# Kernel tuning notes

Hardware: AMD Instinct MI355X
Metric: run time of the kernel (lower is better)

Reference implementation:

```python
import jax, jax.numpy as jnp
import numpy as np

B_, N, C, H = 2048, 49, 384, 12
WH, WW = 7, 7
HEAD_DIM = C // H
SCALE = HEAD_DIM ** -0.5
TABLE = (2 * WH - 1) * (2 * WW - 1)  # 169


def _relative_position_index():
    coords = np.stack(np.meshgrid(np.arange(WH), np.arange(WW), indexing='ij'))  # [2,Wh,Ww]
    flat = coords.reshape(2, -1)  # [2,N]
    rel = flat[:, :, None] - flat[:, None, :]  # [2,N,N]
    rel = rel.transpose(1, 2, 0).astype(np.int32)  # [N,N,2]
    rel[:, :, 0] += WH - 1
    rel[:, :, 1] += WW - 1
    rel[:, :, 0] *= 2 * WW - 1
    return rel.sum(-1)  # [N,N] int32 in [0,169)


def setup_inputs() -> dict:
    key = jax.random.key(0)
    ks = jax.random.split(key, 8)
    return {
        'x': jax.random.normal(ks[0], (B_, N, C), jnp.float32),
        'mask': jax.random.normal(ks[1], (B_, 1, N, N), jnp.float32),
        'stagein': jax.random.uniform(ks[2], (B_, N, C), jnp.float32),
        'rel_bias_table': jax.random.normal(ks[3], (TABLE, H), jnp.float32) * 0.02,
        'rel_pos_index': jnp.asarray(_relative_position_index()),
        'qkv_w': jax.random.normal(ks[4], (3 * C, C), jnp.float32) * 0.02,
        'qkv_b': jax.random.normal(ks[5], (3 * C,), jnp.float32) * 0.02,
        'proj_w': jax.random.normal(ks[6], (C, C), jnp.float32) * 0.02,
        'proj_b': jax.random.normal(ks[7], (C,), jnp.float32) * 0.02,
    }


def reference(x, mask, stagein, rel_bias_table, rel_pos_index, qkv_w, qkv_b, proj_w, proj_b):
    x = x * stagein  # stagein is not None branch
    qkv = x @ qkv_w.T + qkv_b  # [B_, N, 3C]
    qkv = qkv.reshape(B_, N, 3, H, HEAD_DIM).transpose(2, 0, 3, 1, 4)  # [3,B_,H,N,hd]
    q, k, v = qkv[0], qkv[1], qkv[2]
    q = q * SCALE
    attn = jnp.einsum('bhnd,bhmd->bhnm', q, k)  # [B_,H,N,N]
    # relative position bias gather: [N*N] -> [N,N,H] -> [1,H,N,N]
    bias = rel_bias_table[rel_pos_index.reshape(-1)].reshape(N, N, H)
    bias = bias.transpose(2, 0, 1)[None]
    attn = jax.nn.softmax(attn + bias + mask, axis=-1)
    out = jnp.einsum('bhnm,bhmd->bhnd', attn, v)  # [B_,H,N,hd]
    out = out.transpose(0, 2, 1, 3).reshape(B_, N, C)
    return out @ proj_w.T + proj_b
```

## Files before the change

kernel.cpp:

```cpp
#include <hip/hip_runtime.h>
#include <hip/hip_bf16.h>
#include <stdint.h>

#define NWIN 2048
#define NTOK 49
#define CDIM 384
#define NHEAD 12
#define HD 32
#define C3 1152
#define NN2 2401
#define MROWS 100352

typedef __bf16 bf16x8 __attribute__((ext_vector_type(8)));
typedef float f32x4 __attribute__((ext_vector_type(4)));
typedef uint32_t u32x4 __attribute__((ext_vector_type(4)));

static __device__ __forceinline__ unsigned short f2bf(float f) {
  uint32_t u = __builtin_bit_cast(uint32_t, f);
  u += 0x7fffu + ((u >> 16) & 1u);
  return (unsigned short)(u >> 16);
}

static __device__ __forceinline__ void gload_lds16(const void* g, void* l) {
  __builtin_amdgcn_global_load_lds((const __attribute__((address_space(1))) void*)g,
                                   (__attribute__((address_space(3))) void*)l,
                                   16, 0, 0);
}

static __device__ __forceinline__ bf16x8 zero8() {
  u32x4 z = {0u, 0u, 0u, 0u};
  return __builtin_bit_cast(bf16x8, z);
}

__global__ void prep_kernel(const float* __restrict__ qkv_w, const float* __restrict__ proj_w,
                            const float* __restrict__ table, const int* __restrict__ idx,
                            unsigned short* __restrict__ wq, unsigned short* __restrict__ wp,
                            float* __restrict__ biasexp) {
  const int NW1 = C3 * CDIM;
  const int NW2 = CDIM * CDIM;
  const int NB = NHEAD * NN2;
  int i = blockIdx.x * blockDim.x + threadIdx.x;
  int stride = gridDim.x * blockDim.x;
  for (int t = i; t < NW1 + NW2 + NB; t += stride) {
    if (t < NW1) {
      wq[t] = f2bf(qkv_w[t]);
    } else if (t < NW1 + NW2) {
      int j = t - NW1;
      wp[j] = f2bf(proj_w[j]);
    } else {
      int j = t - NW1 - NW2;
      int h = j / NN2;
      int nm = j - h * NN2;
      biasexp[j] = table[idx[nm] * NHEAD + h];
    }
  }
}

__global__ void mul_kernel(const float4* __restrict__ x, const float4* __restrict__ s,
                           u32x4* __restrict__ A, int n8) {
  int i0 = blockIdx.x * blockDim.x + threadIdx.x;
  int stride = gridDim.x * blockDim.x;
  for (int t = i0; t < n8; t += stride) {
    float4 a0 = x[2 * t], a1 = x[2 * t + 1];
    float4 b0 = s[2 * t], b1 = s[2 * t + 1];
    union { unsigned short us[8]; u32x4 v; } o;
    o.us[0] = f2bf(a0.x * b0.x); o.us[1] = f2bf(a0.y * b0.y);
    o.us[2] = f2bf(a0.z * b0.z); o.us[3] = f2bf(a0.w * b0.w);
    o.us[4] = f2bf(a1.x * b1.x); o.us[5] = f2bf(a1.y * b1.y);
    o.us[6] = f2bf(a1.z * b1.z); o.us[7] = f2bf(a1.w * b1.w);
    A[t] = o.v;
  }
}

__launch_bounds__(256, 2)
__global__ void qkv_gemm(const unsigned short* __restrict__ A,
                         const unsigned short* __restrict__ Bw,
                         const float* __restrict__ qkvb,
                         unsigned short* __restrict__ qo,
                         unsigned short* __restrict__ ko,
                         unsigned short* __restrict__ vo) {
  __shared__ unsigned short As[128 * 64];
  __shared__ unsigned short Bs[128 * 64];
  const int tid = threadIdx.x;
  const int w = tid >> 6, l = tid & 63;
  const int l15 = l & 15, lhi = l >> 4;
  const int wgid = (blockIdx.x & 7) * 882 + (blockIdx.x >> 3);
  const int mt = wgid / 9, nt = wgid - mt * 9;
  const int wr = w >> 1, wc = w & 1;
  const int srow = tid >> 3;
  const int scb = (tid & 7) ^ (srow & 7);
  const unsigned short* Ag = A + (size_t)(mt * 128 + srow) * CDIM + scb * 8;
  const unsigned short* Bg = Bw + (size_t)(nt * 128 + srow) * CDIM + scb * 8;
  unsigned short* Asl = As + srow * 64 + (tid & 7) * 8;
  unsigned short* Bsl = Bs + srow * 64 + (tid & 7) * 8;
  const f32x4 z4 = {0.f, 0.f, 0.f, 0.f};
  f32x4 acc[4][4];
#pragma unroll
  for (int m = 0; m < 4; ++m)
#pragma unroll
    for (int n = 0; n < 4; ++n) acc[m][n] = z4;
  const int xr = l15 & 7;
  for (int kt = 0; kt < 6; ++kt) {
    const unsigned short* ag = Ag + kt * 64;
    const unsigned short* bg = Bg + kt * 64;
#pragma unroll
    for (int i = 0; i < 4; ++i) {
      gload_lds16(ag + i * 32 * CDIM, Asl + i * 2048);
      gload_lds16(bg + i * 32 * CDIM, Bsl + i * 2048);
    }
    __syncthreads();
#pragma unroll
    for (int kk = 0; kk < 2; ++kk) {
      const int sl = ((kk << 2) | lhi) ^ xr;
      bf16x8 af[4], bfr[4];
#pragma unroll
      for (int m = 0; m < 4; ++m)
        af[m] = *(const bf16x8*)(As + (wr * 64 + m * 16 + l15) * 64 + sl * 8);
#pragma unroll
      for (int n = 0; n < 4; ++n)
        bfr[n] = *(const bf16x8*)(Bs + (wc * 64 + n * 16 + l15) * 64 + sl * 8);
#pragma unroll
      for (int m = 0; m < 4; ++m)
#pragma unroll
        for (int n = 0; n < 4; ++n)
          acc[m][n] = __builtin_amdgcn_mfma_f32_16x16x32_bf16(af[m], bfr[n], acc[m][n], 0, 0, 0);
    }
    __syncthreads();
  }
  const float SCALE_F = 0.17677669529663687f;
  const int six = nt * 2 + wc;
  const int which = six / 6;
  const int cbase = (six - which * 6) * 64;
  unsigned short* outw = (which == 0) ? qo : ((which == 1) ? ko : vo);
  const float* bptr = qkvb + which * CDIM;
#pragma unroll
  for (int m = 0; m < 4; ++m) {
#pragma unroll
    for (int j = 0; j < 4; ++j) {
      const int r = mt * 128 + wr * 64 + m * 16 + lhi * 4 + j;
      const int bwin = r / 49;
      const int ntok = r - bwin * 49;
#pragma unroll
      for (int n = 0; n < 4; ++n) {
        const int c = cbase + n * 16 + l15;
        const int h = c >> 5, d = c & 31;
        float val = acc[m][n][j] + bptr[c];
        if (which == 0) val *= SCALE_F;
        outw[(((size_t)bwin * NHEAD + h) * NTOK + ntok) * HD + d] = f2bf(val);
      }
    }
  }
}

__launch_bounds__(256, 2)
__global__ void attn_kernel(const unsigned short* __restrict__ q,
                            const unsigned short* __restrict__ kmat,
                            const unsigned short* __restrict__ vmat,
                            const float* __restrict__ mask,
                            const float* __restrict__ biasexp,
                            unsigned short* __restrict__ attnout) {
  __shared__ unsigned short P_lds[4][64 * 72];
  __shared__ unsigned short vT_lds[4][32 * 72];
  const int tid = threadIdx.x;
  const int w = tid >> 6, l = tid & 63;
  const int l15 = l & 15, lhi = l >> 4;
  const int wg = (blockIdx.x & 7) * 768 + (blockIdx.x >> 3);
  const int b = wg / 3, it = wg - b * 3;
  unsigned short* Pw = &P_lds[w][0];
  unsigned short* Vw = &vT_lds[w][0];
  const float* maskb = mask + (size_t)b * NN2;
  const f32x4 z4 = {0.f, 0.f, 0.f, 0.f};
  const int h = it * 4 + w;
  const size_t hb = ((size_t)b * NHEAD + h) * NTOK * HD;
  const unsigned short* qb = q + hb;
  const unsigned short* kb = kmat + hb;
  const unsigned short* vb = vmat + hb;
  {
    const int n = l;
    unsigned short tmp[32];
    if (n < 49) {
      *(u32x4*)(&tmp[0])  = *(const u32x4*)(vb + n * 32);
      *(u32x4*)(&tmp[8])  = *(const u32x4*)(vb + n * 32 + 8);
      *(u32x4*)(&tmp[16]) = *(const u32x4*)(vb + n * 32 + 16);
      *(u32x4*)(&tmp[24]) = *(const u32x4*)(vb + n * 32 + 24);
    } else {
#pragma unroll
      for (int d2 = 0; d2 < 32; ++d2) tmp[d2] = 0;
    }
#pragma unroll
    for (int d2 = 0; d2 < 32; ++d2) Vw[d2 * 72 + n] = tmp[d2];
  }
  bf16x8 aq[4], bk[4];
#pragma unroll
  for (int t = 0; t < 4; ++t) {
    const int row = t * 16 + l15;
    if (row < 49) {
      aq[t] = *(const bf16x8*)(qb + row * 32 + lhi * 8);
      bk[t] = *(const bf16x8*)(kb + row * 32 + lhi * 8);
    } else {
      aq[t] = zero8();
      bk[t] = zero8();
    }
  }
  f32x4 s[4][4];
#pragma unroll
  for (int ti = 0; ti < 4; ++ti)
#pragma unroll
    for (int tj = 0; tj < 4; ++tj)
      s[ti][tj] = __builtin_amdgcn_mfma_f32_16x16x32_bf16(aq[ti], bk[tj], z4, 0, 0, 0);
  const float* biash = biasexp + h * NN2;
#pragma unroll
  for (int ti = 0; ti < 4; ++ti) {
#pragma unroll
    for (int r = 0; r < 4; ++r) {
      const int n = ti * 16 + lhi * 4 + r;
#pragma unroll
      for (int tj = 0; tj < 4; ++tj) {
        const int m = tj * 16 + l15;
        float val = -1e30f;
        if (n < 49 && m < 49)
          val = s[ti][tj][r] + biash[n * 49 + m] + maskb[n * 49 + m];
        s[ti][tj][r] = val;
      }
    }
  }
#pragma unroll
  for (int ti = 0; ti < 4; ++ti) {
#pragma unroll
    for (int r = 0; r < 4; ++r) {
      float mx = fmaxf(fmaxf(s[ti][0][r], s[ti][1][r]), fmaxf(s[ti][2][r], s[ti][3][r]));
      mx = fmaxf(mx, __shfl_xor(mx, 1));
      mx = fmaxf(mx, __shfl_xor(mx, 2));
      mx = fmaxf(mx, __shfl_xor(mx, 4));
      mx = fmaxf(mx, __shfl_xor(mx, 8));
      float e0 = __expf(s[ti][0][r] - mx);
      float e1 = __expf(s[ti][1][r] - mx);
      float e2 = __expf(s[ti][2][r] - mx);
      float e3 = __expf(s[ti][3][r] - mx);
      float sum = (e0 + e1) + (e2 + e3);
      sum += __shfl_xor(sum, 1);
      sum += __shfl_xor(sum, 2);
      sum += __shfl_xor(sum, 4);
      sum += __shfl_xor(sum, 8);
      const float rinv = 1.0f / sum;
      const int n = ti * 16 + lhi * 4 + r;
      unsigned short* pr = Pw + n * 72 + l15;
      pr[0]  = f2bf(e0 * rinv);
      pr[16] = f2bf(e1 * rinv);
      pr[32] = f2bf(e2 * rinv);
      pr[48] = f2bf(e3 * rinv);
    }
  }
  f32x4 o[4][2];
#pragma unroll
  for (int ti = 0; ti < 4; ++ti) { o[ti][0] = z4; o[ti][1] = z4; }
#pragma unroll
  for (int kk = 0; kk < 2; ++kk) {
    bf16x8 pa[4], bv[2];
#pragma unroll
    for (int ti = 0; ti < 4; ++ti)
      pa[ti] = *(const bf16x8*)(Pw + (ti * 16 + l15) * 72 + kk * 32 + lhi * 8);
#pragma unroll
    for (int dj = 0; dj < 2; ++dj)
      bv[dj] = *(const bf16x8*)(Vw + (dj * 16 + l15) * 72 + kk * 32 + lhi * 8);
#pragma unroll
    for (int ti = 0; ti < 4; ++ti)
#pragma unroll
      for (int dj = 0; dj < 2; ++dj)
        o[ti][dj] = __builtin_amdgcn_mfma_f32_16x16x32_bf16(pa[ti], bv[dj], o[ti][dj], 0, 0, 0);
  }
#pragma unroll
  for (int ti = 0; ti < 4; ++ti) {
#pragma unroll
    for (int r = 0; r < 4; ++r) {
      const int n = ti * 16 + lhi * 4 + r;
      if (n < 49) {
        unsigned short* orow = attnout + ((size_t)b * NTOK + n) * CDIM + h * HD;
        orow[l15] = f2bf(o[ti][0][r]);
        orow[16 + l15] = f2bf(o[ti][1][r]);
      }
    }
  }
}

__launch_bounds__(256, 2)
__global__ void proj_gemm(const unsigned short* __restrict__ A,
                          const unsigned short* __restrict__ Bw,
                          const float* __restrict__ pb,
                          float* __restrict__ out) {
  __shared__ unsigned short As[128 * 64];
  __shared__ unsigned short Bs[128 * 64];
  const int tid = threadIdx.x;
  const int w = tid >> 6, l = tid & 63;
  const int l15 = l & 15, lhi = l >> 4;
  const int wgid = (blockIdx.x & 7) * 294 + (blockIdx.x >> 3);
  const int mt = wgid / 3, nt = wgid - mt * 3;
  const int wr = w >> 1, wc = w & 1;
  const int srow = tid >> 3;
  const int scb = (tid & 7) ^ (srow & 7);
  const unsigned short* Ag = A + (size_t)(mt * 128 + srow) * CDIM + scb * 8;
  const unsigned short* Bg = Bw + (size_t)(nt * 128 + srow) * CDIM + scb * 8;
  unsigned short* Asl = As + srow * 64 + (tid & 7) * 8;
  unsigned short* Bsl = Bs + srow * 64 + (tid & 7) * 8;
  const f32x4 z4 = {0.f, 0.f, 0.f, 0.f};
  f32x4 acc[4][4];
#pragma unroll
  for (int m = 0; m < 4; ++m)
#pragma unroll
    for (int n = 0; n < 4; ++n) acc[m][n] = z4;
  const int xr = l15 & 7;
  for (int kt = 0; kt < 6; ++kt) {
    const unsigned short* ag = Ag + kt * 64;
    const unsigned short* bg = Bg + kt * 64;
#pragma unroll
    for (int i = 0; i < 4; ++i) {
      gload_lds16(ag + i * 32 * CDIM, Asl + i * 2048);
      gload_lds16(bg + i * 32 * CDIM, Bsl + i * 2048);
    }
    __syncthreads();
#pragma unroll
    for (int kk = 0; kk < 2; ++kk) {
      const int sl = ((kk << 2) | lhi) ^ xr;
      bf16x8 af[4], bfr[4];
#pragma unroll
      for (int m = 0; m < 4; ++m)
        af[m] = *(const bf16x8*)(As + (wr * 64 + m * 16 + l15) * 64 + sl * 8);
#pragma unroll
      for (int n = 0; n < 4; ++n)
        bfr[n] = *(const bf16x8*)(Bs + (wc * 64 + n * 16 + l15) * 64 + sl * 8);
#pragma unroll
      for (int m = 0; m < 4; ++m)
#pragma unroll
        for (int n = 0; n < 4; ++n)
          acc[m][n] = __builtin_amdgcn_mfma_f32_16x16x32_bf16(af[m], bfr[n], acc[m][n], 0, 0, 0);
    }
    __syncthreads();
  }
#pragma unroll
  for (int m = 0; m < 4; ++m) {
#pragma unroll
    for (int j = 0; j < 4; ++j) {
      const int r = mt * 128 + wr * 64 + m * 16 + lhi * 4 + j;
      float* orow = out + (size_t)r * CDIM;
#pragma unroll
      for (int n = 0; n < 4; ++n) {
        const int c = nt * 128 + wc * 64 + n * 16 + l15;
        orow[c] = acc[m][n][j] + pb[c];
      }
    }
  }
}

extern "C" void kernel_launch(void* const* d_in, const int* in_sizes, int n_in,
                              void* d_out, int out_size, void* d_ws, size_t ws_size,
                              hipStream_t stream) {
  const float* x       = (const float*)d_in[0];
  const float* mask    = (const float*)d_in[1];
  const float* stagein = (const float*)d_in[2];
  const float* table   = (const float*)d_in[3];
  const int*   idx     = (const int*)d_in[4];
  const float* qkv_w   = (const float*)d_in[5];
  const float* qkv_b   = (const float*)d_in[6];
  const float* proj_w  = (const float*)d_in[7];
  const float* proj_b  = (const float*)d_in[8];
  float* out = (float*)d_out;
  char* ws = (char*)d_ws;

  const size_t SZA = (size_t)MROWS * CDIM * 2;
  unsigned short* Abf = (unsigned short*)(ws);
  unsigned short* qb  = (unsigned short*)(ws + SZA);
  unsigned short* kb  = (unsigned short*)(ws + 2 * SZA);
  unsigned short* vb  = (unsigned short*)(ws + 3 * SZA);
  unsigned short* wq  = (unsigned short*)(ws + 4 * SZA);
  unsigned short* wp  = (unsigned short*)(ws + 4 * SZA + (size_t)C3 * CDIM * 2);
  float* biasexp      = (float*)(ws + 4 * SZA + (size_t)C3 * CDIM * 2 + (size_t)CDIM * CDIM * 2);
  unsigned short* attnout = Abf;

  prep_kernel<<<dim3(512), dim3(256), 0, stream>>>(qkv_w, proj_w, table, idx, wq, wp, biasexp);
  mul_kernel<<<dim3(2048), dim3(256), 0, stream>>>((const float4*)x, (const float4*)stagein,
                                                   (u32x4*)Abf, MROWS * CDIM / 8);
  qkv_gemm<<<dim3(784 * 9), dim3(256), 0, stream>>>(Abf, wq, qkv_b, qb, kb, vb);
  attn_kernel<<<dim3(NWIN * 3), dim3(256), 0, stream>>>(qb, kb, vb, mask, biasexp, attnout);
  proj_gemm<<<dim3(784 * 3), dim3(256), 0, stream>>>(attnout, wp, proj_b, out);
}
```

Measured before the change: 477.6 us.

## Compute transposed scores in attention and keep P in registers via shuffles

Attention scores are computed as K·Q^T so each query row lies in one lane column, which cuts the softmax reduction to two cross-lane shuffles. The softmax probabilities are packed to bf16 in registers and redistributed with shuffles into the MFMA operand layout, removing the P LDS buffer and its stores and loads. To keep bias and mask reads coalesced in the new layout, the bias table is expanded transposed and a new kernel writes a transposed copy of the mask. This adds an extra full read and write of the mask tensor in exchange for a lighter attention kernel.

New measurement: 422.0 us. -11.6%, faster.

```diff
diff --git a/kernel.cpp b/kernel.cpp
--- a/kernel.cpp
+++ b/kernel.cpp
@@ -14,6 +14,7 @@
 typedef __bf16 bf16x8 __attribute__((ext_vector_type(8)));
 typedef float f32x4 __attribute__((ext_vector_type(4)));
 typedef uint32_t u32x4 __attribute__((ext_vector_type(4)));
+typedef unsigned int u32;
 
 static __device__ __forceinline__ unsigned short f2bf(float f) {
   uint32_t u = __builtin_bit_cast(uint32_t, f);
@@ -21,6 +22,10 @@
   return (unsigned short)(u >> 16);
 }
 
+static __device__ __forceinline__ u32 pk2(float a, float b) {
+  return (u32)f2bf(a) | ((u32)f2bf(b) << 16);
+}
+
 static __device__ __forceinline__ void gload_lds16(const void* g, void* l) {
   __builtin_amdgcn_global_load_lds((const __attribute__((address_space(1))) void*)g,
                                    (__attribute__((address_space(3))) void*)l,
@@ -35,7 +40,7 @@
 __global__ void prep_kernel(const float* __restrict__ qkv_w, const float* __restrict__ proj_w,
                             const float* __restrict__ table, const int* __restrict__ idx,
                             unsigned short* __restrict__ wq, unsigned short* __restrict__ wp,
-                            float* __restrict__ biasexp) {
+                            float* __restrict__ biasT) {
   const int NW1 = C3 * CDIM;
   const int NW2 = CDIM * CDIM;
   const int NB = NHEAD * NN2;
@@ -51,8 +56,20 @@
       int j = t - NW1 - NW2;
       int h = j / NN2;
       int nm = j - h * NN2;
-      biasexp[j] = table[idx[nm] * NHEAD + h];
-    }
+      int m = nm / 49, n = nm - m * 49;
+      biasT[j] = table[idx[n * 49 + m] * NHEAD + h];
+    }
+  }
+}
+
+__global__ void maskT_kernel(const float* __restrict__ mask, float* __restrict__ maskT) {
+  __shared__ float t[NN2];
+  const int b = blockIdx.x;
+  for (int i = threadIdx.x; i < NN2; i += 256) t[i] = mask[(size_t)b * NN2 + i];
+  __syncthreads();
+  for (int i = threadIdx.x; i < NN2; i += 256) {
+    int m = i / 49, n = i - m * 49;
+    maskT[(size_t)b * NN2 + i] = t[n * 49 + m];
   }
 }
 
@@ -156,19 +173,17 @@
 __global__ void attn_kernel(const unsigned short* __restrict__ q,
                             const unsigned short* __restrict__ kmat,
                             const unsigned short* __restrict__ vmat,
-                            const float* __restrict__ mask,
-                            const float* __restrict__ biasexp,
+                            const float* __restrict__ maskT,
+                            const float* __restrict__ biasT,
                             unsigned short* __restrict__ attnout) {
-  __shared__ unsigned short P_lds[4][64 * 72];
   __shared__ unsigned short vT_lds[4][32 * 72];
   const int tid = threadIdx.x;
   const int w = tid >> 6, l = tid & 63;
   const int l15 = l & 15, lhi = l >> 4;
   const int wg = (blockIdx.x & 7) * 768 + (blockIdx.x >> 3);
   const int b = wg / 3, it = wg - b * 3;
-  unsigned short* Pw = &P_lds[w][0];
   unsigned short* Vw = &vT_lds[w][0];
-  const float* maskb = mask + (size_t)b * NN2;
+  const float* maskb = maskT + (size_t)b * NN2;
   const f32x4 z4 = {0.f, 0.f, 0.f, 0.f};
   const int h = it * 4 + w;
   const size_t hb = ((size_t)b * NHEAD + h) * NTOK * HD;
@@ -202,72 +217,79 @@
       bk[t] = zero8();
     }
   }
-  f32x4 s[4][4];
-#pragma unroll
-  for (int ti = 0; ti < 4; ++ti)
-#pragma unroll
-    for (int tj = 0; tj < 4; ++tj)
-      s[ti][tj] = __builtin_amdgcn_mfma_f32_16x16x32_bf16(aq[ti], bk[tj], z4, 0, 0, 0);
-  const float* biash = biasexp + h * NN2;
-#pragma unroll
-  for (int ti = 0; ti < 4; ++ti) {
-#pragma unroll
-    for (int r = 0; r < 4; ++r) {
-      const int n = ti * 16 + lhi * 4 + r;
-#pragma unroll
-      for (int tj = 0; tj < 4; ++tj) {
-        const int m = tj * 16 + l15;
+  const float* biash = biasT + h * NN2;
+  u32 P4[4][4][2];
+#pragma unroll
+  for (int nt = 0; nt < 4; ++nt) {
+    f32x4 s4[4];
+#pragma unroll
+    for (int mt = 0; mt < 4; ++mt)
+      s4[mt] = __builtin_amdgcn_mfma_f32_16x16x32_bf16(bk[mt], aq[nt], z4, 0, 0, 0);
+    const int n = nt * 16 + l15;
+#pragma unroll
+    for (int mt = 0; mt < 4; ++mt) {
+#pragma unroll
+      for (int r = 0; r < 4; ++r) {
+        const int m = mt * 16 + lhi * 4 + r;
         float val = -1e30f;
         if (n < 49 && m < 49)
-          val = s[ti][tj][r] + biash[n * 49 + m] + maskb[n * 49 + m];
-        s[ti][tj][r] = val;
+          val = s4[mt][r] + biash[m * 49 + n] + maskb[m * 49 + n];
+        s4[mt][r] = val;
       }
     }
-  }
-#pragma unroll
-  for (int ti = 0; ti < 4; ++ti) {
-#pragma unroll
-    for (int r = 0; r < 4; ++r) {
-      float mx = fmaxf(fmaxf(s[ti][0][r], s[ti][1][r]), fmaxf(s[ti][2][r], s[ti][3][r]));
-      mx = fmaxf(mx, __shfl_xor(mx, 1));
-      mx = fmaxf(mx, __shfl_xor(mx, 2));
-      mx = fmaxf(mx, __shfl_xor(mx, 4));
-      mx = fmaxf(mx, __shfl_xor(mx, 8));
-      float e0 = __expf(s[ti][0][r] - mx);
-      float e1 = __expf(s[ti][1][r] - mx);
-      float e2 = __expf(s[ti][2][r] - mx);
-      float e3 = __expf(s[ti][3][r] - mx);
-      float sum = (e0 + e1) + (e2 + e3);
-      sum += __shfl_xor(sum, 1);
-      sum += __shfl_xor(sum, 2);
-      sum += __shfl_xor(sum, 4);
-      sum += __shfl_xor(sum, 8);
-      const float rinv = 1.0f / sum;
-      const int n = ti * 16 + lhi * 4 + r;
-      unsigned short* pr = Pw + n * 72 + l15;
-      pr[0]  = f2bf(e0 * rinv);
-      pr[16] = f2bf(e1 * rinv);
-      pr[32] = f2bf(e2 * rinv);
-      pr[48] = f2bf(e3 * rinv);
-    }
-  }
+    float mx = s4[0][0];
+#pragma unroll
+    for (int mt = 0; mt < 4; ++mt)
+#pragma unroll
+      for (int r = 0; r < 4; ++r) mx = fmaxf(mx, s4[mt][r]);
+    mx = fmaxf(mx, __shfl_xor(mx, 16));
+    mx = fmaxf(mx, __shfl_xor(mx, 32));
+    float sum = 0.f;
+#pragma unroll
+    for (int mt = 0; mt < 4; ++mt)
+#pragma unroll
+      for (int r = 0; r < 4; ++r) {
+        s4[mt][r] = __expf(s4[mt][r] - mx);
+        sum += s4[mt][r];
+      }
+    sum += __shfl_xor(sum, 16);
+    sum += __shfl_xor(sum, 32);
+    const float rinv = 1.0f / sum;
+#pragma unroll
+    for (int mt = 0; mt < 4; ++mt) {
+      P4[nt][mt][0] = pk2(s4[mt][0] * rinv, s4[mt][1] * rinv);
+      P4[nt][mt][1] = pk2(s4[mt][2] * rinv, s4[mt][3] * rinv);
+    }
+  }
+  const int sA = ((l >> 4) & 1) * 32 + l15;
+  const int sB = sA + 16;
+  const bool hi_sel = (l & 32) != 0;
   f32x4 o[4][2];
 #pragma unroll
   for (int ti = 0; ti < 4; ++ti) { o[ti][0] = z4; o[ti][1] = z4; }
 #pragma unroll
   for (int kk = 0; kk < 2; ++kk) {
-    bf16x8 pa[4], bv[2];
-#pragma unroll
-    for (int ti = 0; ti < 4; ++ti)
-      pa[ti] = *(const bf16x8*)(Pw + (ti * 16 + l15) * 72 + kk * 32 + lhi * 8);
-#pragma unroll
-    for (int dj = 0; dj < 2; ++dj)
-      bv[dj] = *(const bf16x8*)(Vw + (dj * 16 + l15) * 72 + kk * 32 + lhi * 8);
-#pragma unroll
-    for (int ti = 0; ti < 4; ++ti)
-#pragma unroll
-      for (int dj = 0; dj < 2; ++dj)
-        o[ti][dj] = __builtin_amdgcn_mfma_f32_16x16x32_bf16(pa[ti], bv[dj], o[ti][dj], 0, 0, 0);
+    bf16x8 bv0 = *(const bf16x8*)(Vw + l15 * 72 + kk * 32 + lhi * 8);
+    bf16x8 bv1 = *(const bf16x8*)(Vw + (16 + l15) * 72 + kk * 32 + lhi * 8);
+#pragma unroll
+    for (int ti = 0; ti < 4; ++ti) {
+      int x0 = __shfl((int)P4[ti][2 * kk][0], sA);
+      int x1 = __shfl((int)P4[ti][2 * kk][1], sA);
+      int y0 = __shfl((int)P4[ti][2 * kk + 1][0], sA);
+      int y1 = __shfl((int)P4[ti][2 * kk + 1][1], sA);
+      int x2 = __shfl((int)P4[ti][2 * kk][0], sB);
+      int x3 = __shfl((int)P4[ti][2 * kk][1], sB);
+      int y2 = __shfl((int)P4[ti][2 * kk + 1][0], sB);
+      int y3 = __shfl((int)P4[ti][2 * kk + 1][1], sB);
+      u32x4 f;
+      f[0] = (u32)(hi_sel ? y0 : x0);
+      f[1] = (u32)(hi_sel ? y1 : x1);
+      f[2] = (u32)(hi_sel ? y2 : x2);
+      f[3] = (u32)(hi_sel ? y3 : x3);
+      bf16x8 pa = __builtin_bit_cast(bf16x8, f);
+      o[ti][0] = __builtin_amdgcn_mfma_f32_16x16x32_bf16(pa, bv0, o[ti][0], 0, 0, 0);
+      o[ti][1] = __builtin_amdgcn_mfma_f32_16x16x32_bf16(pa, bv1, o[ti][1], 0, 0, 0);
+    }
   }
 #pragma unroll
   for (int ti = 0; ti < 4; ++ti) {
@@ -373,13 +395,15 @@
   unsigned short* vb  = (unsigned short*)(ws + 3 * SZA);
   unsigned short* wq  = (unsigned short*)(ws + 4 * SZA);
   unsigned short* wp  = (unsigned short*)(ws + 4 * SZA + (size_t)C3 * CDIM * 2);
-  float* biasexp      = (float*)(ws + 4 * SZA + (size_t)C3 * CDIM * 2 + (size_t)CDIM * CDIM * 2);
+  float* biasT        = (float*)(ws + 4 * SZA + (size_t)C3 * CDIM * 2 + (size_t)CDIM * CDIM * 2);
+  float* maskT        = biasT + (size_t)NHEAD * NN2;
   unsigned short* attnout = Abf;
 
-  prep_kernel<<<dim3(512), dim3(256), 0, stream>>>(qkv_w, proj_w, table, idx, wq, wp, biasexp);
+  prep_kernel<<<dim3(512), dim3(256), 0, stream>>>(qkv_w, proj_w, table, idx, wq, wp, biasT);
+  maskT_kernel<<<dim3(NWIN), dim3(256), 0, stream>>>(mask, maskT);
   mul_kernel<<<dim3(2048), dim3(256), 0, stream>>>((const float4*)x, (const float4*)stagein,
                                                    (u32x4*)Abf, MROWS * CDIM / 8);
   qkv_gemm<<<dim3(784 * 9), dim3(256), 0, stream>>>(Abf, wq, qkv_b, qb, kb, vb);
-  attn_kernel<<<dim3(NWIN * 3), dim3(256), 0, stream>>>(qb, kb, vb, mask, biasexp, attnout);
+  attn_kernel<<<dim3(NWIN * 3), dim3(256), 0, stream>>>(qb, kb, vb, maskT, biasT, attnout);
   proj_gemm<<<dim3(784 * 3), dim3(256), 0, stream>>>(attnout, wp, proj_b, out);
 }
```
